# Kernel optimization log

Measured on AMD Instinct MI355X. Metric: run time of the kernel, lower is better.

Reference implementation:

```python
import jax, jax.numpy as jnp
import numpy as np
import math

D = 4096            # input dim and all hidden dims
TOKENS = (4, 2048)  # batch, seq
P = 0.8             # excitatory fraction for EI layers


def conn_dense(kernel, x):
    # bool kernel interpreted as +1 (True) / -1 (False)
    w = jnp.where(kernel, jnp.asarray(1.0, x.dtype), jnp.asarray(-1.0, x.dtype))
    return x @ w


def ei_dense(x, kernel, scale, p):
    in_dim = x.shape[-1]
    ne = round(in_dim * p)  # excitatory count
    x_exc = x[..., :ne]
    x_inh = x[..., ne:]
    xx = jnp.concatenate([x_exc, (-p / (1.0 - p)) * x_inh], axis=-1)
    return scale * conn_dense(kernel, xx)


def setup_inputs() -> dict:
    key = jax.random.key(0)
    ks = jax.random.split(key, 4)
    x = jax.random.normal(ks[0], (*TOKENS, D), dtype=jnp.float32)
    k0 = jax.random.bernoulli(ks[1], 0.5, (D, D))
    k1 = jax.random.bernoulli(ks[2], 0.5, (D, D))
    k2 = jax.random.bernoulli(ks[3], 0.5, (D, D))
    s = jnp.asarray(1.0 / math.sqrt(D), dtype=jnp.float32)
    return {"x": x, "k0": k0, "s0": s, "k1": k1, "s1": s, "k2": k2, "s2": s}


def reference(x, k0, s0, k1, s1, k2, s2):
    # layer 0: Dense_01 (plain +/-1 matmul, scale), then relu*2
    h = s0 * conn_dense(k0, x)
    h = jax.nn.relu(h) * 2.0
    # layer 1: Dense_EI, then relu*2
    h = ei_dense(h, k1, s1, P)
    h = jax.nn.relu(h) * 2.0
    # layer 2: Dense_EI (no activation on last layer)
    return ei_dense(h, k2, s2, P)
```

## Files before the change

### kernel.cpp

```cpp
#include <hip/hip_runtime.h>
#include <stdint.h>

#define DD 4096
#define NE_IDX 3277

typedef __attribute__((ext_vector_type(8))) short short8;
typedef __attribute__((ext_vector_type(4))) float f32x4;
typedef __attribute__((ext_vector_type(16))) float f32x16;
typedef __attribute__((ext_vector_type(4))) unsigned int u32x4;

__device__ __forceinline__ unsigned short f2bf(float f) {
    unsigned int u = __float_as_uint(f);
    u += 0x7fffu + ((u >> 16) & 1u);
    return (unsigned short)(u >> 16);
}

__device__ __forceinline__ void gload16(const void* g, void* l) {
    __builtin_amdgcn_global_load_lds(
        (const __attribute__((address_space(1))) unsigned int*)g,
        (__attribute__((address_space(3))) unsigned int*)l,
        16, 0, 0);
}

__global__ void detect_kernel(const unsigned int* __restrict__ k0, int* __restrict__ flag) {
    if (blockIdx.x == 0 && threadIdx.x == 0) {
        int ok4 = 1;
        for (int i = 0; i < 256; ++i) {
            unsigned int v = k0[i];
            if (!(v == 0u || v == 1u || v == 0x3f800000u)) { ok4 = 0; break; }
        }
        *flag = ok4;
    }
}

__global__ void pack_x_kernel(const float* __restrict__ x, unsigned short* __restrict__ xb, int n8) {
    const int stride = gridDim.x * blockDim.x;
    for (int i = blockIdx.x * blockDim.x + threadIdx.x; i < n8; i += stride) {
        const float4* p = (const float4*)(x + (size_t)i * 8);
        float4 a = p[0], b = p[1];
        short8 r;
        r[0] = (short)f2bf(a.x); r[1] = (short)f2bf(a.y);
        r[2] = (short)f2bf(a.z); r[3] = (short)f2bf(a.w);
        r[4] = (short)f2bf(b.x); r[5] = (short)f2bf(b.y);
        r[6] = (short)f2bf(b.z); r[7] = (short)f2bf(b.w);
        *(short8*)(xb + (size_t)i * 8) = r;
    }
}

__global__ void pack_w_kernel(const void* __restrict__ kin, unsigned short* __restrict__ wt,
                              const float* __restrict__ sptr, float inh, int ne,
                              const int* __restrict__ flag) {
    __shared__ unsigned short tile[64][68];
    const int elem4 = *flag;
    const float s = *sptr;
    const int i0 = blockIdx.x * 64;
    const int j0 = blockIdx.y * 64;
    const int t = threadIdx.x;
    {
        const int il = t >> 2;
        const int jc = (t & 3) * 16;
        const int gi = i0 + il;
        const float mag = s * ((gi < ne) ? 1.0f : inh);
        const unsigned short pos = f2bf(mag);
        const unsigned short neg = f2bf(-mag);
        if (elem4) {
            const unsigned int* k32 = (const unsigned int*)kin + (size_t)gi * DD + j0 + jc;
            #pragma unroll
            for (int q = 0; q < 4; ++q) {
                u32x4 v = *(const u32x4*)(k32 + q * 4);
                #pragma unroll
                for (int e = 0; e < 4; ++e)
                    tile[il][jc + q * 4 + e] = v[e] ? pos : neg;
            }
        } else {
            const unsigned char* k8 = (const unsigned char*)kin + (size_t)gi * DD + j0 + jc;
            u32x4 v = *(const u32x4*)k8;
            #pragma unroll
            for (int q = 0; q < 4; ++q) {
                unsigned int w = v[q];
                tile[il][jc + q * 4 + 0] = (w & 0xffu) ? pos : neg;
                tile[il][jc + q * 4 + 1] = ((w >> 8) & 0xffu) ? pos : neg;
                tile[il][jc + q * 4 + 2] = ((w >> 16) & 0xffu) ? pos : neg;
                tile[il][jc + q * 4 + 3] = ((w >> 24) & 0xffu) ? pos : neg;
            }
        }
    }
    __syncthreads();
    {
        const int jl = t >> 2;
        const int ic = (t & 3) * 16;
        short8 o0, o1;
        #pragma unroll
        for (int e = 0; e < 8; ++e) o0[e] = (short)tile[ic + e][jl];
        #pragma unroll
        for (int e = 0; e < 8; ++e) o1[e] = (short)tile[ic + 8 + e][jl];
        unsigned short* dst = wt + (size_t)(j0 + jl) * DD + i0 + ic;
        *(short8*)(dst) = o0;
        *(short8*)(dst + 8) = o1;
    }
}

#define PH32(MH, NH, LA, LB, STAGE_STMT, EB) do {                               \
    if (LA) {                                                                   \
        _Pragma("unroll")                                                       \
        for (int mi = 0; mi < 2; ++mi)                                          \
            _Pragma("unroll")                                                   \
            for (int s = 0; s < 4; ++s)                                         \
                af[mi][s] = *(const short8*)(Lc + (abh[(MH)*2+mi] ^ (s<<5)));   \
    }                                                                           \
    if (LB) {                                                                   \
        _Pragma("unroll")                                                       \
        for (int s = 0; s < 4; ++s)                                             \
            bf[s] = *(const short8*)(Lc + (bbh[(NH)] ^ (s<<5)));                \
    }                                                                           \
    STAGE_STMT;                                                                 \
    asm volatile("s_waitcnt vmcnt(4)" ::: "memory");                            \
    __builtin_amdgcn_s_barrier();                                               \
    asm volatile("s_waitcnt lgkmcnt(0)" ::: "memory");                          \
    __builtin_amdgcn_sched_barrier(0);                                          \
    __builtin_amdgcn_s_setprio(1);                                              \
    _Pragma("unroll")                                                           \
    for (int s = 0; s < 4; ++s)                                                 \
        _Pragma("unroll")                                                       \
        for (int mi = 0; mi < 2; ++mi)                                          \
            acc[(MH)*2+mi][(NH)] = __builtin_amdgcn_mfma_f32_32x32x16_bf16(     \
                af[mi][s], bf[s], acc[(MH)*2+mi][(NH)], 0, 0, 0);               \
    __builtin_amdgcn_s_setprio(0);                                              \
    __builtin_amdgcn_sched_barrier(0);                                          \
    if (EB) __builtin_amdgcn_s_barrier();                                       \
} while (0)

template <int MODE>
__global__ __launch_bounds__(512, 2)
void gemm256_kernel(const unsigned short* __restrict__ A,
                    const unsigned short* __restrict__ Bt,
                    void* __restrict__ Cout)
{
    __shared__ unsigned short L[65536];
    const char* Lc = (const char*)L;

    const int tid  = threadIdx.x;
    const int lane = tid & 63;
    const int l31  = lane & 31;
    const int hb   = lane >> 5;
    const int wave = tid >> 6;
    const int wr   = wave >> 2;
    const int wc   = wave & 3;

    int wg = blockIdx.x;
    const int per = gridDim.x >> 3;
    wg = (wg & 7) * per + (wg >> 3);
    const int tm = wg >> 4;
    const int tn = wg & 15;

    const size_t arow0 = (size_t)tm * 256;
    const size_t brow0 = (size_t)tn * 256;

    const int rq = tid >> 3;
    const int wq = (tid >> 6) << 3;
    const int srcoff = (((tid & 7) ^ ((tid >> 3) & 7)) << 3);

    auto stageA = [&](int sb, int c, int kt) {
        #pragma unroll
        for (int q = 0; q < 2; ++q) {
            const int dr = c * 64 + q * 128 + rq;
            gload16(A + ((arow0 + dr) << 12) + kt + srcoff,
                    (void*)&L[sb + ((c * 64 + q * 128 + wq) << 6)]);
        }
    };
    auto stageB = [&](int sb, int c, int kt) {
        #pragma unroll
        for (int q = 0; q < 2; ++q) {
            const int lr  = q * 64 + rq;
            const int dr  = c * 32 + (lr & 31) + (lr >> 5) * 64;
            const int wlr = q * 64 + wq;
            const int wdr = c * 32 + (wlr & 31) + (wlr >> 5) * 64;
            gload16(Bt + ((brow0 + dr) << 12) + kt + srcoff,
                    (void*)&L[sb + 16384 + (wdr << 6)]);
        }
    };

    int abh[4], bbh[2];
    #pragma unroll
    for (int mt = 0; mt < 4; ++mt) {
        const int r = wr * 128 + mt * 32 + l31;
        abh[mt] = r * 128 + ((hb ^ (r & 7)) << 4);
    }
    #pragma unroll
    for (int nt = 0; nt < 2; ++nt) {
        const int r = wc * 64 + nt * 32 + l31;
        bbh[nt] = 32768 + r * 128 + ((hb ^ (r & 7)) << 4);
    }

    short8 af[2][4], bf[4];
    f32x16 acc[4][2];
    #pragma unroll
    for (int m = 0; m < 4; ++m)
        #pragma unroll
        for (int n = 0; n < 2; ++n)
            #pragma unroll
            for (int e = 0; e < 16; ++e)
                acc[m][n][e] = 0.f;

    stageA(0, 0, 0); stageB(0, 0, 0); stageB(0, 1, 0); stageA(0, 1, 0);
    asm volatile("s_waitcnt vmcnt(4)" ::: "memory");
    __builtin_amdgcn_s_barrier();
    __builtin_amdgcn_sched_barrier(0);

    for (int t = 0; t < 63; ++t) {
        const int sb  = ((t & 1) ^ 1) * 32768;
        const int kt1 = (t + 1) * 64;
        PH32(0, 0, 1, 1, stageA(sb, 0, kt1), 0);
        PH32(0, 1, 0, 1, stageB(sb, 0, kt1), 0);
        PH32(1, 1, 1, 0, stageB(sb, 1, kt1), 0);
        PH32(1, 0, 0, 1, stageA(sb, 1, kt1), 1);
        #pragma unroll
        for (int i = 0; i < 4; ++i) abh[i] ^= 65536;
        bbh[0] ^= 65536; bbh[1] ^= 65536;
    }
    asm volatile("s_waitcnt vmcnt(0)" ::: "memory");
    __builtin_amdgcn_s_barrier();
    __builtin_amdgcn_sched_barrier(0);
    PH32(0, 0, 1, 1, (void)0, 0);
    PH32(0, 1, 0, 1, (void)0, 0);
    PH32(1, 1, 1, 0, (void)0, 0);
    PH32(1, 0, 0, 1, (void)0, 0);

    const int orow0 = tm * 256 + wr * 128 + hb * 4;
    const int ocol0 = tn * 256 + wc * 64 + l31;
    #pragma unroll
    for (int mt = 0; mt < 4; ++mt) {
        #pragma unroll
        for (int nt = 0; nt < 2; ++nt) {
            #pragma unroll
            for (int reg = 0; reg < 16; ++reg) {
                const int row = orow0 + mt * 32 + (reg & 3) + 8 * (reg >> 2);
                const int col = ocol0 + nt * 32;
                float v = acc[mt][nt][reg];
                if (MODE == 1) {
                    v = fmaxf(v, 0.0f) * 2.0f;
                    ((unsigned short*)Cout)[((size_t)row << 12) + col] = f2bf(v);
                } else {
                    ((float*)Cout)[((size_t)row << 12) + col] = v;
                }
            }
        }
    }
}

extern "C" void kernel_launch(void* const* d_in, const int* in_sizes, int n_in,
                              void* d_out, int out_size, void* d_ws, size_t ws_size,
                              hipStream_t stream) {
    const float* x  = (const float*)d_in[0];
    const void*  k0 = d_in[1];
    const float* s0 = (const float*)d_in[2];
    const void*  k1 = d_in[3];
    const float* s1 = (const float*)d_in[4];
    const void*  k2 = d_in[5];
    const float* s2 = (const float*)d_in[6];

    const int M = in_sizes[0] / DD;

    const size_t act_bytes = (size_t)M * DD * 2;
    const size_t w_bytes   = (size_t)DD * DD * 2;
    const size_t need      = act_bytes * 2 + w_bytes + 256;
    if (ws_size < need) return;

    char* ws = (char*)d_ws;
    unsigned short* xb = (unsigned short*)ws;
    unsigned short* h1 = (unsigned short*)(ws + act_bytes);
    unsigned short* wt = (unsigned short*)(ws + act_bytes * 2);
    int* flag          = (int*)(ws + act_bytes * 2 + w_bytes);

    detect_kernel<<<1, 64, 0, stream>>>((const unsigned int*)k0, flag);
    pack_x_kernel<<<2048, 256, 0, stream>>>(x, xb, M * DD / 8);

    dim3 pw_grid(DD / 64, DD / 64);
    const int gemm_grid = (M / 256) * (DD / 256);

    pack_w_kernel<<<pw_grid, 256, 0, stream>>>(k0, wt, s0, 1.0f, DD, flag);
    gemm256_kernel<1><<<gemm_grid, 512, 0, stream>>>(xb, wt, h1);

    pack_w_kernel<<<pw_grid, 256, 0, stream>>>(k1, wt, s1, -4.0f, NE_IDX, flag);
    gemm256_kernel<1><<<gemm_grid, 512, 0, stream>>>(h1, wt, xb);

    pack_w_kernel<<<pw_grid, 256, 0, stream>>>(k2, wt, s2, -4.0f, NE_IDX, flag);
    gemm256_kernel<0><<<gemm_grid, 512, 0, stream>>>(xb, wt, (float*)d_out);
}
```

Measured before the change: 766.2 us.

## Re-lay LDS tiles as paired-row 256B lines and keep both B fragments in registers

Changes the LDS tile layout so that two consecutive rows share a 256-byte line, with a 16-slot XOR swizzle. Global-to-LDS staging addresses and the fragment read offsets are recomputed to match, with the aim of cutting LDS bank conflicts on the MFMA operand reads. The B fragments are also held for both N halves (bf[2][4]), which lets the last phase reuse the B registers loaded earlier instead of reloading them from LDS. The cost is more VGPRs, which could hurt occupancy at 512 threads with 2 blocks per CU.

New measurement: 733.5 us. -4.3%, faster.

```diff
diff --git a/kernel.cpp b/kernel.cpp
--- a/kernel.cpp
+++ b/kernel.cpp
@@ -5,7 +5,6 @@
 #define NE_IDX 3277
 
 typedef __attribute__((ext_vector_type(8))) short short8;
-typedef __attribute__((ext_vector_type(4))) float f32x4;
 typedef __attribute__((ext_vector_type(16))) float f32x16;
 typedef __attribute__((ext_vector_type(4))) unsigned int u32x4;
 
@@ -106,12 +105,12 @@
         for (int mi = 0; mi < 2; ++mi)                                          \
             _Pragma("unroll")                                                   \
             for (int s = 0; s < 4; ++s)                                         \
-                af[mi][s] = *(const short8*)(Lc + (abh[(MH)*2+mi] ^ (s<<5)));   \
+                af[mi][s] = *(const short8*)(Lc + (ab2[(MH)*2+mi] ^ (s<<5)));   \
     }                                                                           \
     if (LB) {                                                                   \
         _Pragma("unroll")                                                       \
         for (int s = 0; s < 4; ++s)                                             \
-            bf[s] = *(const short8*)(Lc + (bbh[(NH)] ^ (s<<5)));                \
+            bf[(NH)][s] = *(const short8*)(Lc + (bb2[(NH)] ^ (s<<5)));          \
     }                                                                           \
     STAGE_STMT;                                                                 \
     asm volatile("s_waitcnt vmcnt(4)" ::: "memory");                            \
@@ -124,7 +123,7 @@
         _Pragma("unroll")                                                       \
         for (int mi = 0; mi < 2; ++mi)                                          \
             acc[(MH)*2+mi][(NH)] = __builtin_amdgcn_mfma_f32_32x32x16_bf16(     \
-                af[mi][s], bf[s], acc[(MH)*2+mi][(NH)], 0, 0, 0);               \
+                af[mi][s], bf[(NH)][s], acc[(MH)*2+mi][(NH)], 0, 0, 0);         \
     __builtin_amdgcn_s_setprio(0);                                              \
     __builtin_amdgcn_sched_barrier(0);                                          \
     if (EB) __builtin_amdgcn_s_barrier();                                       \
@@ -156,43 +155,44 @@
     const size_t arow0 = (size_t)tm * 256;
     const size_t brow0 = (size_t)tn * 256;
 
-    const int rq = tid >> 3;
-    const int wq = (tid >> 6) << 3;
-    const int srcoff = (((tid & 7) ^ ((tid >> 3) & 7)) << 3);
+    const int sx  = (tid & 15) ^ ((tid >> 4) & 15);
+    const int kcS = (sx & 7) << 3;
+    const int rbS = sx >> 3;
+    const int arowloc = ((tid >> 4) << 1) + rbS;
+    const int lcl = tid & 255;
+    const int seg = tid >> 8;
+    const int browloc = ((lcl >> 4) << 1) + rbS;
 
     auto stageA = [&](int sb, int c, int kt) {
         #pragma unroll
         for (int q = 0; q < 2; ++q) {
-            const int dr = c * 64 + q * 128 + rq;
-            gload16(A + ((arow0 + dr) << 12) + kt + srcoff,
-                    (void*)&L[sb + ((c * 64 + q * 128 + wq) << 6)]);
+            gload16(A + ((arow0 + c * 64 + q * 128 + arowloc) << 12) + kt + kcS,
+                    (void*)&L[sb + (c * 32 + q * 64) * 128 + tid * 8]);
         }
     };
     auto stageB = [&](int sb, int c, int kt) {
         #pragma unroll
         for (int q = 0; q < 2; ++q) {
-            const int lr  = q * 64 + rq;
-            const int dr  = c * 32 + (lr & 31) + (lr >> 5) * 64;
-            const int wlr = q * 64 + wq;
-            const int wdr = c * 32 + (wlr & 31) + (wlr >> 5) * 64;
-            gload16(Bt + ((brow0 + dr) << 12) + kt + srcoff,
-                    (void*)&L[sb + 16384 + (wdr << 6)]);
+            const int d0 = c * 16 + seg * 32 + q * 64;
+            gload16(Bt + ((brow0 + d0 * 2 + browloc) << 12) + kt + kcS,
+                    (void*)&L[sb + 16384 + d0 * 128 + lcl * 8]);
         }
     };
 
-    int abh[4], bbh[2];
+    const int slot0 = (hb | ((l31 & 1) << 3)) ^ (l31 >> 1);
+    int ab2[4], bb2[2];
     #pragma unroll
     for (int mt = 0; mt < 4; ++mt) {
-        const int r = wr * 128 + mt * 32 + l31;
-        abh[mt] = r * 128 + ((hb ^ (r & 7)) << 4);
+        const int d = wr * 64 + mt * 16 + (l31 >> 1);
+        ab2[mt] = (d << 8) + (slot0 << 4);
     }
     #pragma unroll
     for (int nt = 0; nt < 2; ++nt) {
-        const int r = wc * 64 + nt * 32 + l31;
-        bbh[nt] = 32768 + r * 128 + ((hb ^ (r & 7)) << 4);
-    }
-
-    short8 af[2][4], bf[4];
+        const int d = wc * 32 + nt * 16 + (l31 >> 1);
+        bb2[nt] = 32768 + (d << 8) + (slot0 << 4);
+    }
+
+    short8 af[2][4], bf[2][4];
     f32x16 acc[4][2];
     #pragma unroll
     for (int m = 0; m < 4; ++m)
@@ -213,10 +213,10 @@
         PH32(0, 0, 1, 1, stageA(sb, 0, kt1), 0);
         PH32(0, 1, 0, 1, stageB(sb, 0, kt1), 0);
         PH32(1, 1, 1, 0, stageB(sb, 1, kt1), 0);
-        PH32(1, 0, 0, 1, stageA(sb, 1, kt1), 1);
-        #pragma unroll
-        for (int i = 0; i < 4; ++i) abh[i] ^= 65536;
-        bbh[0] ^= 65536; bbh[1] ^= 65536;
+        PH32(1, 0, 0, 0, stageA(sb, 1, kt1), 1);
+        #pragma unroll
+        for (int i = 0; i < 4; ++i) ab2[i] ^= 65536;
+        bb2[0] ^= 65536; bb2[1] ^= 65536;
     }
     asm volatile("s_waitcnt vmcnt(0)" ::: "memory");
     __builtin_amdgcn_s_barrier();
@@ -224,7 +224,7 @@
     PH32(0, 0, 1, 1, (void)0, 0);
     PH32(0, 1, 0, 1, (void)0, 0);
     PH32(1, 1, 1, 0, (void)0, 0);
-    PH32(1, 0, 0, 1, (void)0, 0);
+    PH32(1, 0, 0, 0, (void)0, 0);
 
     const int orow0 = tm * 256 + wr * 128 + hb * 4;
     const int ocol0 = tn * 256 + wc * 64 + l31;
```
